# Kernel optimization log

Measured on AMD Instinct MI355X. Metric: run time of the kernel, lower is better.

The kernel has to match this reference:

```python
import jax, jax.numpy as jnp
import numpy as np

N = 4096
D = 256
H = 8
E = 131072
NEG = -1e30  # stands in for -inf; keeps grads NaN-free


def setup_inputs() -> dict:
    key = jax.random.key(0)
    ks = jax.random.split(key, 8)
    s = 1.0 / np.sqrt(D)
    return {
        "x": jax.random.normal(ks[0], (N, D), dtype=jnp.float32),
        "edge_index": jax.random.randint(ks[1], (2, E), 0, N, dtype=jnp.int32),
        "Wq": jax.random.normal(ks[2], (D, D), dtype=jnp.float32) * s,
        "Wk": jax.random.normal(ks[3], (D, D), dtype=jnp.float32) * s,
        "Wv": jax.random.normal(ks[4], (D, D), dtype=jnp.float32) * s,
        "Wo": jax.random.normal(ks[5], (D, D), dtype=jnp.float32) * s,
        "bo": jnp.zeros((D,), dtype=jnp.float32),
        "gamma": jnp.ones((D,), dtype=jnp.float32),
        "beta": jnp.zeros((D,), dtype=jnp.float32),
    }


def reference(x, edge_index, Wq, Wk, Wv, Wo, bo, gamma, beta):
    n, d_model = x.shape
    d_h = d_model // H
    scale = jnp.sqrt(jnp.float32(d_h))

    # mask: True = blocked. Diagonal and graph edges (dst attends to src) unblocked.
    mask = jnp.ones((n, n), dtype=bool)
    diag = jnp.arange(n)
    mask = mask.at[diag, diag].set(False)
    src, dst = edge_index[0], edge_index[1]
    mask = mask.at[dst, src].set(False)

    # projections: torch Linear computes x @ W.T
    Q = (x @ Wq.T).reshape(n, H, d_h).transpose(1, 0, 2)  # [H, N, d_h]
    K = (x @ Wk.T).reshape(n, H, d_h).transpose(1, 0, 2)
    V = (x @ Wv.T).reshape(n, H, d_h).transpose(1, 0, 2)

    scores = jnp.einsum("hnd,hmd->hnm", Q, K) / scale      # [H, N, N]
    scores = jnp.where(mask[None, :, :], NEG, scores)
    attn = jax.nn.softmax(scores, axis=-1)
    attn = jnp.nan_to_num(attn, nan=0.0)

    out = jnp.einsum("hnm,hmd->hnd", attn, V)              # [H, N, d_h]
    out = out.transpose(1, 0, 2).reshape(n, d_model)
    out = out @ Wo.T + bo

    # LayerNorm(x + out), eps=1e-5
    h = x + out
    mu = jnp.mean(h, axis=-1, keepdims=True)
    var = jnp.var(h, axis=-1, keepdims=True)
    return (h - mu) * jax.lax.rsqrt(var + 1e-5) * gamma + beta
```

## Files before the change

kernel.cpp:

```cpp
#include <hip/hip_runtime.h>

#define D_MODEL 256
#define N_HEADS 8
#define MAXN 128
#define NGEMM 384

typedef __attribute__((ext_vector_type(8))) short bf16x8;
typedef __attribute__((ext_vector_type(4))) float f32x4;

#define WSYNC() asm volatile("s_waitcnt lgkmcnt(0)" ::: "memory")

__device__ __forceinline__ unsigned short f2bf(float f) {
    union { float f; unsigned int u; } v; v.f = f;
    unsigned int r = v.u + 0x7fff + ((v.u >> 16) & 1);
    return (unsigned short)(r >> 16);
}
__device__ __forceinline__ float bf2f(unsigned short u) {
    union { unsigned int u; float f; } v; v.u = ((unsigned int)u) << 16;
    return v.f;
}

__global__ void prep_kernel(const float* __restrict__ x,
                            const float* __restrict__ W0, const float* __restrict__ W1,
                            const float* __restrict__ W2, const float* __restrict__ W3,
                            unsigned short* __restrict__ xb,
                            unsigned short* __restrict__ O0, unsigned short* __restrict__ O1,
                            unsigned short* __restrict__ O2, unsigned short* __restrict__ O3,
                            unsigned long long* __restrict__ mask, int n) {
    const int XV = (4096 * 256) / 4;
    int i = blockIdx.x * blockDim.x + threadIdx.x;

    int wpr = n >> 6;
    int mwords = n * wpr;
    if (i < mwords) {
        int row = i >> 6;
        int w = i & 63;
        mask[i] = (w == (row >> 6)) ? (1ULL << (row & 63)) : 0ULL;
    }

    const float* src;
    unsigned short* dst;
    int k;
    if (i < XV) {
        src = x; dst = xb; k = i;
    } else {
        int i2 = i - XV;
        if (i2 >= 4 * 16384) return;
        int z = i2 >> 14;
        k = i2 & 16383;
        src = (z == 0) ? W0 : (z == 1) ? W1 : (z == 2) ? W2 : W3;
        dst = (z == 0) ? O0 : (z == 1) ? O1 : (z == 2) ? O2 : O3;
    }
    float4 v = *(const float4*)(src + (size_t)k * 4);
    ushort4 o;
    o.x = f2bf(v.x); o.y = f2bf(v.y); o.z = f2bf(v.z); o.w = f2bf(v.w);
    *(ushort4*)(dst + (size_t)k * 4) = o;
}

__global__ __launch_bounds__(256) void qkv_edges_kernel(
        const unsigned short* __restrict__ xb,
        const unsigned short* __restrict__ Wq, const unsigned short* __restrict__ Wk,
        const unsigned short* __restrict__ Wv,
        unsigned short* __restrict__ Qb, unsigned short* __restrict__ Kb,
        unsigned short* __restrict__ Vb,
        const int* __restrict__ ei, unsigned long long* __restrict__ mask,
        int E, int n) {
    int blk = blockIdx.x;
    if (blk >= NGEMM) {
        int e = (blk - NGEMM) * 256 + threadIdx.x;
        if (e < E) {
            int src = ei[e];
            int dst = ei[E + e];
            int wpr = n >> 6;
            atomicOr(&mask[(size_t)dst * wpr + (src >> 6)], 1ULL << (src & 63));
        }
        return;
    }
    int z = blk >> 7;
    int r = blk & 127;
    int by = r >> 2, bx = r & 3;
    const unsigned short* B = (z == 0) ? Wq : (z == 1) ? Wk : Wv;
    unsigned short* Cb = (z == 0) ? Qb : (z == 1) ? Kb : Vb;

    __shared__ short Alds[128][72];
    __shared__ short Blds[64][72];
    int t = threadIdx.x;
    int wave = t >> 6, lane = t & 63;
    int wr = wave >> 1, wc = wave & 1;
    int lr = t >> 3;
    int lk = (t & 7) << 3;

    const unsigned short* Abase = xb + ((size_t)(by * 128 + lr)) * D_MODEL + lk;
    const unsigned short* Bbase = B + ((size_t)(bx * 64 + lr)) * D_MODEL + lk;

    int fm = lane & 15;
    int fk = (lane >> 4) << 3;

    f32x4 acc[4][2];
#pragma unroll
    for (int rr = 0; rr < 4; ++rr)
#pragma unroll
        for (int c = 0; c < 2; ++c) acc[rr][c] = (f32x4){0.f, 0.f, 0.f, 0.f};

    for (int k0 = 0; k0 < D_MODEL; k0 += 64) {
        *(uint4*)&Alds[lr][lk]      = *(const uint4*)(Abase + k0);
        *(uint4*)&Alds[lr + 32][lk] = *(const uint4*)(Abase + 32 * D_MODEL + k0);
        *(uint4*)&Alds[lr + 64][lk] = *(const uint4*)(Abase + 64 * D_MODEL + k0);
        *(uint4*)&Alds[lr + 96][lk] = *(const uint4*)(Abase + 96 * D_MODEL + k0);
        *(uint4*)&Blds[lr][lk]      = *(const uint4*)(Bbase + k0);
        *(uint4*)&Blds[lr + 32][lk] = *(const uint4*)(Bbase + 32 * D_MODEL + k0);
        __syncthreads();
#pragma unroll
        for (int ks = 0; ks < 64; ks += 32) {
            bf16x8 af[4], bf[2];
#pragma unroll
            for (int rr = 0; rr < 4; ++rr)
                af[rr] = *(const bf16x8*)&Alds[wr * 64 + rr * 16 + fm][ks + fk];
#pragma unroll
            for (int c = 0; c < 2; ++c)
                bf[c] = *(const bf16x8*)&Blds[wc * 32 + c * 16 + fm][ks + fk];
#pragma unroll
            for (int rr = 0; rr < 4; ++rr)
#pragma unroll
                for (int c = 0; c < 2; ++c)
                    acc[rr][c] = __builtin_amdgcn_mfma_f32_16x16x32_bf16(
                        af[rr], bf[c], acc[rr][c], 0, 0, 0);
        }
        __syncthreads();
    }

    int orow0 = by * 128 + wr * 64 + ((lane >> 4) << 2);
    int ocol0 = bx * 64 + wc * 32 + (lane & 15);
#pragma unroll
    for (int rr = 0; rr < 4; ++rr)
#pragma unroll
        for (int c = 0; c < 2; ++c)
#pragma unroll
            for (int q = 0; q < 4; ++q)
                Cb[(size_t)(orow0 + rr * 16 + q) * D_MODEL + ocol0 + c * 16] =
                    f2bf(acc[rr][c][q]);
}

__global__ __launch_bounds__(256, 8) void attn_kernel(
        const unsigned short* __restrict__ Qb, const unsigned short* __restrict__ Kb,
        const unsigned short* __restrict__ Vb,
        const unsigned long long* __restrict__ mask,
        unsigned short* __restrict__ Ob, int n) {
    __shared__ int nbr_s[4][MAXN + 16];
    __shared__ float s_s[4][N_HEADS][MAXN];

    int t = threadIdx.x;
    int wave = t >> 6, L = t & 63;
    int wpr = n >> 6;
    int dst = blockIdx.x * 4 + wave;

    int* nbrw = nbr_s[wave];
    float (*sw)[MAXN] = s_s[wave];

    unsigned long long w = (L < wpr) ? mask[(size_t)dst * wpr + L] : 0ULL;
    int c = __popcll(w);
    int xs = c;
#pragma unroll
    for (int o = 1; o < 64; o <<= 1) {
        int y = __shfl_up(xs, o, 64);
        if (L >= o) xs += y;
    }
    int pos = xs - c;
    while (w) {
        int b = __builtin_ctzll(w);
        w &= w - 1;
        if (pos < MAXN) nbrw[pos] = (L << 6) + b;
        ++pos;
    }
    int cnt = __shfl(xs, 63, 64);
    if (cnt > MAXN) cnt = MAXN;
    int nb = (cnt + 15) & ~15;
    WSYNC();
    int last = nbrw[cnt - 1];
    if (L < nb - cnt) nbrw[cnt + L] = last;
    WSYNC();

    int col = L & 15;
    int kq = L >> 4;
    bf16x8 qf = (bf16x8){0, 0, 0, 0, 0, 0, 0, 0};
    if (col < N_HEADS)
        qf = *(const bf16x8*)(Qb + (size_t)dst * D_MODEL + col * 32 + kq * 8);
    const bf16x8 zf = (bf16x8){0, 0, 0, 0, 0, 0, 0, 0};
    const float inv_scale = 0.17677669529663687f;

    for (int b0 = 0; b0 < nb; b0 += 16) {
        int nj = nbrw[b0 + col];
        const unsigned short* krow = Kb + (size_t)nj * D_MODEL + kq * 8;
        f32x4 c0 = (f32x4){0.f, 0.f, 0.f, 0.f};
        f32x4 c1 = (f32x4){0.f, 0.f, 0.f, 0.f};
#pragma unroll
        for (int kb = 0; kb < 8; kb += 2) {
            bf16x8 a0 = *(const bf16x8*)(krow + kb * 32);
            bf16x8 a1 = *(const bf16x8*)(krow + kb * 32 + 32);
            bf16x8 bop0 = (col == kb)     ? qf : zf;
            bf16x8 bop1 = (col == kb + 1) ? qf : zf;
            c0 = __builtin_amdgcn_mfma_f32_16x16x32_bf16(a0, bop0, c0, 0, 0, 0);
            c1 = __builtin_amdgcn_mfma_f32_16x16x32_bf16(a1, bop1, c1, 0, 0, 0);
        }
        if (col < N_HEADS) {
            int jr = b0 + kq * 4;
            float4 o4;
            float s0 = (c0[0] + c1[0]) * inv_scale;
            float s1 = (c0[1] + c1[1]) * inv_scale;
            float s2 = (c0[2] + c1[2]) * inv_scale;
            float s3 = (c0[3] + c1[3]) * inv_scale;
            o4.x = (jr + 0 < cnt) ? s0 : -1e30f;
            o4.y = (jr + 1 < cnt) ? s1 : -1e30f;
            o4.z = (jr + 2 < cnt) ? s2 : -1e30f;
            o4.w = (jr + 3 < cnt) ? s3 : -1e30f;
            *(float4*)&sw[col][jr] = o4;
        }
    }
    WSYNC();

    int h = L >> 3, li = L & 7;
    float m = -1e30f;
    for (int j0 = li * 4; j0 < nb; j0 += 32) {
        float4 v = *(const float4*)&sw[h][j0];
        m = fmaxf(m, fmaxf(fmaxf(v.x, v.y), fmaxf(v.z, v.w)));
    }
    m = fmaxf(m, __shfl_xor(m, 1, 8));
    m = fmaxf(m, __shfl_xor(m, 2, 8));
    m = fmaxf(m, __shfl_xor(m, 4, 8));
    float l = 0.f;
    for (int j0 = li * 4; j0 < nb; j0 += 32) {
        float4 v = *(const float4*)&sw[h][j0];
        float4 e4;
        e4.x = __expf(v.x - m); e4.y = __expf(v.y - m);
        e4.z = __expf(v.z - m); e4.w = __expf(v.w - m);
        *(float4*)&sw[h][j0] = e4;
        l += (e4.x + e4.y) + (e4.z + e4.w);
    }
    l += __shfl_xor(l, 1, 8);
    l += __shfl_xor(l, 2, 8);
    l += __shfl_xor(l, 4, 8);
    WSYNC();

    f32x4 acc = (f32x4){0.f, 0.f, 0.f, 0.f};
    const unsigned short* vb = Vb + 4 * L;
    for (int j = 0; j < nb; j += 4) {
        float4 wv = *(const float4*)&sw[h][j];
        int j0 = nbrw[j], j1 = nbrw[j + 1], j2 = nbrw[j + 2], j3 = nbrw[j + 3];
        uint2 r0 = *(const uint2*)(vb + (size_t)j0 * D_MODEL);
        uint2 r1 = *(const uint2*)(vb + (size_t)j1 * D_MODEL);
        uint2 r2 = *(const uint2*)(vb + (size_t)j2 * D_MODEL);
        uint2 r3 = *(const uint2*)(vb + (size_t)j3 * D_MODEL);
        acc[0] += wv.x * bf2f((unsigned short)(r0.x & 0xffff));
        acc[1] += wv.x * bf2f((unsigned short)(r0.x >> 16));
        acc[2] += wv.x * bf2f((unsigned short)(r0.y & 0xffff));
        acc[3] += wv.x * bf2f((unsigned short)(r0.y >> 16));
        acc[0] += wv.y * bf2f((unsigned short)(r1.x & 0xffff));
        acc[1] += wv.y * bf2f((unsigned short)(r1.x >> 16));
        acc[2] += wv.y * bf2f((unsigned short)(r1.y & 0xffff));
        acc[3] += wv.y * bf2f((unsigned short)(r1.y >> 16));
        acc[0] += wv.z * bf2f((unsigned short)(r2.x & 0xffff));
        acc[1] += wv.z * bf2f((unsigned short)(r2.x >> 16));
        acc[2] += wv.z * bf2f((unsigned short)(r2.y & 0xffff));
        acc[3] += wv.z * bf2f((unsigned short)(r2.y >> 16));
        acc[0] += wv.w * bf2f((unsigned short)(r3.x & 0xffff));
        acc[1] += wv.w * bf2f((unsigned short)(r3.x >> 16));
        acc[2] += wv.w * bf2f((unsigned short)(r3.y & 0xffff));
        acc[3] += wv.w * bf2f((unsigned short)(r3.y >> 16));
    }
    float rl = 1.f / l;
    ushort4 o;
    o.x = f2bf(acc[0] * rl); o.y = f2bf(acc[1] * rl);
    o.z = f2bf(acc[2] * rl); o.w = f2bf(acc[3] * rl);
    *(ushort4*)(Ob + (size_t)dst * D_MODEL + 4 * L) = o;
    WSYNC();
}

struct SMemO {
    union {
        struct { short A[32][72]; short B[256][72]; } st;
        float c[32][260];
    };
};

__global__ __launch_bounds__(256) void gemm_o_ln_kernel(
        const unsigned short* __restrict__ Ob, const unsigned short* __restrict__ Wob,
        const float* __restrict__ x, const float* __restrict__ bo,
        const float* __restrict__ gamma, const float* __restrict__ beta,
        float* __restrict__ out) {
    __shared__ SMemO sm;
    int by = blockIdx.x;
    int t = threadIdx.x;
    int wave = t >> 6, lane = t & 63;
    int rt = wave >> 1, cq = wave & 1;
    int lr = t >> 3;
    int lk = (t & 7) << 3;

    const unsigned short* Abase = Ob + ((size_t)(by * 32 + lr)) * D_MODEL + lk;
    int fm = lane & 15;
    int fk = (lane >> 4) << 3;

    f32x4 acc[8];
#pragma unroll
    for (int ct = 0; ct < 8; ++ct) acc[ct] = (f32x4){0.f, 0.f, 0.f, 0.f};

    for (int k0 = 0; k0 < D_MODEL; k0 += 64) {
        *(uint4*)&sm.st.A[lr][lk] = *(const uint4*)(Abase + k0);
#pragma unroll
        for (int j = 0; j < 8; ++j)
            *(uint4*)&sm.st.B[lr + 32 * j][lk] =
                *(const uint4*)(Wob + ((size_t)(lr + 32 * j)) * D_MODEL + k0 + lk);
        __syncthreads();
#pragma unroll
        for (int ks = 0; ks < 64; ks += 32) {
            bf16x8 af = *(const bf16x8*)&sm.st.A[rt * 16 + fm][ks + fk];
#pragma unroll
            for (int ct = 0; ct < 8; ++ct) {
                bf16x8 bf = *(const bf16x8*)&sm.st.B[cq * 128 + ct * 16 + fm][ks + fk];
                acc[ct] = __builtin_amdgcn_mfma_f32_16x16x32_bf16(af, bf, acc[ct], 0, 0, 0);
            }
        }
        __syncthreads();
    }

    int rr0 = rt * 16 + ((lane >> 4) << 2);
#pragma unroll
    for (int ct = 0; ct < 8; ++ct)
#pragma unroll
        for (int q = 0; q < 4; ++q)
            sm.c[rr0 + q][cq * 128 + ct * 16 + (lane & 15)] = acc[ct][q];
    __syncthreads();

    float4 bo4 = *(const float4*)(bo + lane * 4);
    float4 g4  = *(const float4*)(gamma + lane * 4);
    float4 be4 = *(const float4*)(beta + lane * 4);
#pragma unroll
    for (int rr = 0; rr < 8; ++rr) {
        int r = wave * 8 + rr;
        int grow = by * 32 + r;
        float4 p = *(const float4*)&sm.c[r][lane * 4];
        float4 xv = *(const float4*)(x + (size_t)grow * D_MODEL + lane * 4);
        float hx = p.x + xv.x + bo4.x;
        float hy = p.y + xv.y + bo4.y;
        float hz = p.z + xv.z + bo4.z;
        float hw = p.w + xv.w + bo4.w;
        float s  = (hx + hy) + (hz + hw);
        float s2 = (hx * hx + hy * hy) + (hz * hz + hw * hw);
#pragma unroll
        for (int o = 32; o; o >>= 1) {
            s  += __shfl_xor(s, o, 64);
            s2 += __shfl_xor(s2, o, 64);
        }
        float mu = s * (1.f / 256.f);
        float var = s2 * (1.f / 256.f) - mu * mu;
        float rstd = rsqrtf(var + 1e-5f);
        float4 o4;
        o4.x = (hx - mu) * rstd * g4.x + be4.x;
        o4.y = (hy - mu) * rstd * g4.y + be4.y;
        o4.z = (hz - mu) * rstd * g4.z + be4.z;
        o4.w = (hw - mu) * rstd * g4.w + be4.w;
        *(float4*)(out + (size_t)grow * D_MODEL + lane * 4) = o4;
    }
}

extern "C" void kernel_launch(void* const* d_in, const int* in_sizes, int n_in,
                              void* d_out, int out_size, void* d_ws, size_t ws_size,
                              hipStream_t stream) {
    const float* x     = (const float*)d_in[0];
    const int*   ei    = (const int*)  d_in[1];
    const float* Wq    = (const float*)d_in[2];
    const float* Wk    = (const float*)d_in[3];
    const float* Wv    = (const float*)d_in[4];
    const float* Wo    = (const float*)d_in[5];
    const float* bo    = (const float*)d_in[6];
    const float* gamma = (const float*)d_in[7];
    const float* beta  = (const float*)d_in[8];
    float* out = (float*)d_out;

    int n = in_sizes[0] / D_MODEL;
    int E = in_sizes[1] / 2;

    char* ws = (char*)d_ws;
    size_t off = 0;
    unsigned long long* mask = (unsigned long long*)(ws + off);
    off += (size_t)n * (n >> 6) * sizeof(unsigned long long);
    unsigned short* xb  = (unsigned short*)(ws + off); off += (size_t)n * D_MODEL * 2;
    unsigned short* Wqb = (unsigned short*)(ws + off); off += D_MODEL * D_MODEL * 2;
    unsigned short* Wkb = (unsigned short*)(ws + off); off += D_MODEL * D_MODEL * 2;
    unsigned short* Wvb = (unsigned short*)(ws + off); off += D_MODEL * D_MODEL * 2;
    unsigned short* Wob = (unsigned short*)(ws + off); off += D_MODEL * D_MODEL * 2;
    unsigned short* Qb  = (unsigned short*)(ws + off); off += (size_t)n * D_MODEL * 2;
    unsigned short* Kb  = (unsigned short*)(ws + off); off += (size_t)n * D_MODEL * 2;
    unsigned short* Vb  = (unsigned short*)(ws + off); off += (size_t)n * D_MODEL * 2;
    unsigned short* Ob  = (unsigned short*)(ws + off); off += (size_t)n * D_MODEL * 2;

    prep_kernel<<<1280, 256, 0, stream>>>(x, Wq, Wk, Wv, Wo,
                                          xb, Wqb, Wkb, Wvb, Wob, mask, n);

    int edge_blocks = (E + 255) / 256;
    qkv_edges_kernel<<<NGEMM + edge_blocks, 256, 0, stream>>>(
        xb, Wqb, Wkb, Wvb, Qb, Kb, Vb, ei, mask, E, n);

    attn_kernel<<<n / 4, 256, 0, stream>>>(Qb, Kb, Vb, mask, Ob, n);

    gemm_o_ln_kernel<<<n / 32, 256, 0, stream>>>(Ob, Wob, x, bo, gamma, beta, out);
}
```

Measured before the change: 114.1 us.

## Retile QKV and output GEMMs and restructure attention gather loops

The QKV GEMM now stages 128-wide K slices, so it runs half as many k-iterations and barriers. In the attention kernel, all eight K fragments are loaded up front and spread across four MFMA accumulators to shorten the dependency chain. The V gather now uses 16-byte loads, with two half-waves each taking alternate neighbours and combining through a cross-lane shuffle, and occupancy hints are lowered. The output GEMM+LayerNorm uses 16-row tiles to double the block count, at the cost of reloading Wo into LDS more often overall.

```diff
diff --git a/kernel.cpp b/kernel.cpp
--- a/kernel.cpp
+++ b/kernel.cpp
@@ -82,16 +82,13 @@
     const unsigned short* B = (z == 0) ? Wq : (z == 1) ? Wk : Wv;
     unsigned short* Cb = (z == 0) ? Qb : (z == 1) ? Kb : Vb;
 
-    __shared__ short Alds[128][72];
-    __shared__ short Blds[64][72];
+    __shared__ short Alds[128][136];
+    __shared__ short Blds[64][136];
     int t = threadIdx.x;
     int wave = t >> 6, lane = t & 63;
     int wr = wave >> 1, wc = wave & 1;
-    int lr = t >> 3;
-    int lk = (t & 7) << 3;
-
-    const unsigned short* Abase = xb + ((size_t)(by * 128 + lr)) * D_MODEL + lk;
-    const unsigned short* Bbase = B + ((size_t)(bx * 64 + lr)) * D_MODEL + lk;
+    int lrA = t >> 4;
+    int lc = (t & 15) << 3;
 
     int fm = lane & 15;
     int fk = (lane >> 4) << 3;
@@ -102,16 +99,18 @@
 #pragma unroll
         for (int c = 0; c < 2; ++c) acc[rr][c] = (f32x4){0.f, 0.f, 0.f, 0.f};
 
-    for (int k0 = 0; k0 < D_MODEL; k0 += 64) {
-        *(uint4*)&Alds[lr][lk]      = *(const uint4*)(Abase + k0);
-        *(uint4*)&Alds[lr + 32][lk] = *(const uint4*)(Abase + 32 * D_MODEL + k0);
-        *(uint4*)&Alds[lr + 64][lk] = *(const uint4*)(Abase + 64 * D_MODEL + k0);
-        *(uint4*)&Alds[lr + 96][lk] = *(const uint4*)(Abase + 96 * D_MODEL + k0);
-        *(uint4*)&Blds[lr][lk]      = *(const uint4*)(Bbase + k0);
-        *(uint4*)&Blds[lr + 32][lk] = *(const uint4*)(Bbase + 32 * D_MODEL + k0);
+    for (int k0 = 0; k0 < D_MODEL; k0 += 128) {
+#pragma unroll
+        for (int i = 0; i < 8; ++i)
+            *(uint4*)&Alds[lrA + 16 * i][lc] =
+                *(const uint4*)(xb + ((size_t)(by * 128 + lrA + 16 * i)) * D_MODEL + k0 + lc);
+#pragma unroll
+        for (int i = 0; i < 4; ++i)
+            *(uint4*)&Blds[lrA + 16 * i][lc] =
+                *(const uint4*)(B + ((size_t)(bx * 64 + lrA + 16 * i)) * D_MODEL + k0 + lc);
         __syncthreads();
 #pragma unroll
-        for (int ks = 0; ks < 64; ks += 32) {
+        for (int ks = 0; ks < 128; ks += 32) {
             bf16x8 af[4], bf[2];
 #pragma unroll
             for (int rr = 0; rr < 4; ++rr)
@@ -141,13 +140,14 @@
                     f2bf(acc[rr][c][q]);
 }
 
-__global__ __launch_bounds__(256, 8) void attn_kernel(
+__global__ __launch_bounds__(256, 4) void attn_kernel(
         const unsigned short* __restrict__ Qb, const unsigned short* __restrict__ Kb,
         const unsigned short* __restrict__ Vb,
         const unsigned long long* __restrict__ mask,
         unsigned short* __restrict__ Ob, int n) {
     __shared__ int nbr_s[4][MAXN + 16];
     __shared__ float s_s[4][N_HEADS][MAXN];
+    __shared__ float lsum_s[4][N_HEADS];
 
     int t = threadIdx.x;
     int wave = t >> 6, L = t & 63;
@@ -191,24 +191,29 @@
     for (int b0 = 0; b0 < nb; b0 += 16) {
         int nj = nbrw[b0 + col];
         const unsigned short* krow = Kb + (size_t)nj * D_MODEL + kq * 8;
+        bf16x8 a[8];
+#pragma unroll
+        for (int kb = 0; kb < 8; ++kb)
+            a[kb] = *(const bf16x8*)(krow + kb * 32);
         f32x4 c0 = (f32x4){0.f, 0.f, 0.f, 0.f};
         f32x4 c1 = (f32x4){0.f, 0.f, 0.f, 0.f};
-#pragma unroll
-        for (int kb = 0; kb < 8; kb += 2) {
-            bf16x8 a0 = *(const bf16x8*)(krow + kb * 32);
-            bf16x8 a1 = *(const bf16x8*)(krow + kb * 32 + 32);
-            bf16x8 bop0 = (col == kb)     ? qf : zf;
-            bf16x8 bop1 = (col == kb + 1) ? qf : zf;
-            c0 = __builtin_amdgcn_mfma_f32_16x16x32_bf16(a0, bop0, c0, 0, 0, 0);
-            c1 = __builtin_amdgcn_mfma_f32_16x16x32_bf16(a1, bop1, c1, 0, 0, 0);
-        }
+        f32x4 c2 = (f32x4){0.f, 0.f, 0.f, 0.f};
+        f32x4 c3 = (f32x4){0.f, 0.f, 0.f, 0.f};
+        c0 = __builtin_amdgcn_mfma_f32_16x16x32_bf16(a[0], (col == 0) ? qf : zf, c0, 0, 0, 0);
+        c1 = __builtin_amdgcn_mfma_f32_16x16x32_bf16(a[1], (col == 1) ? qf : zf, c1, 0, 0, 0);
+        c2 = __builtin_amdgcn_mfma_f32_16x16x32_bf16(a[2], (col == 2) ? qf : zf, c2, 0, 0, 0);
+        c3 = __builtin_amdgcn_mfma_f32_16x16x32_bf16(a[3], (col == 3) ? qf : zf, c3, 0, 0, 0);
+        c0 = __builtin_amdgcn_mfma_f32_16x16x32_bf16(a[4], (col == 4) ? qf : zf, c0, 0, 0, 0);
+        c1 = __builtin_amdgcn_mfma_f32_16x16x32_bf16(a[5], (col == 5) ? qf : zf, c1, 0, 0, 0);
+        c2 = __builtin_amdgcn_mfma_f32_16x16x32_bf16(a[6], (col == 6) ? qf : zf, c2, 0, 0, 0);
+        c3 = __builtin_amdgcn_mfma_f32_16x16x32_bf16(a[7], (col == 7) ? qf : zf, c3, 0, 0, 0);
         if (col < N_HEADS) {
             int jr = b0 + kq * 4;
             float4 o4;
-            float s0 = (c0[0] + c1[0]) * inv_scale;
-            float s1 = (c0[1] + c1[1]) * inv_scale;
-            float s2 = (c0[2] + c1[2]) * inv_scale;
-            float s3 = (c0[3] + c1[3]) * inv_scale;
+            float s0 = ((c0[0] + c1[0]) + (c2[0] + c3[0])) * inv_scale;
+            float s1 = ((c0[1] + c1[1]) + (c2[1] + c3[1])) * inv_scale;
+            float s2 = ((c0[2] + c1[2]) + (c2[2] + c3[2])) * inv_scale;
+            float s3 = ((c0[3] + c1[3]) + (c2[3] + c3[3])) * inv_scale;
             o4.x = (jr + 0 < cnt) ? s0 : -1e30f;
             o4.y = (jr + 1 < cnt) ? s1 : -1e30f;
             o4.z = (jr + 2 < cnt) ? s2 : -1e30f;
@@ -239,46 +244,57 @@
     l += __shfl_xor(l, 1, 8);
     l += __shfl_xor(l, 2, 8);
     l += __shfl_xor(l, 4, 8);
+    if (li == 0) lsum_s[wave][h] = l;
     WSYNC();
 
-    f32x4 acc = (f32x4){0.f, 0.f, 0.f, 0.f};
-    const unsigned short* vb = Vb + 4 * L;
-    for (int j = 0; j < nb; j += 4) {
-        float4 wv = *(const float4*)&sw[h][j];
-        int j0 = nbrw[j], j1 = nbrw[j + 1], j2 = nbrw[j + 2], j3 = nbrw[j + 3];
-        uint2 r0 = *(const uint2*)(vb + (size_t)j0 * D_MODEL);
-        uint2 r1 = *(const uint2*)(vb + (size_t)j1 * D_MODEL);
-        uint2 r2 = *(const uint2*)(vb + (size_t)j2 * D_MODEL);
-        uint2 r3 = *(const uint2*)(vb + (size_t)j3 * D_MODEL);
-        acc[0] += wv.x * bf2f((unsigned short)(r0.x & 0xffff));
-        acc[1] += wv.x * bf2f((unsigned short)(r0.x >> 16));
-        acc[2] += wv.x * bf2f((unsigned short)(r0.y & 0xffff));
-        acc[3] += wv.x * bf2f((unsigned short)(r0.y >> 16));
-        acc[0] += wv.y * bf2f((unsigned short)(r1.x & 0xffff));
-        acc[1] += wv.y * bf2f((unsigned short)(r1.x >> 16));
-        acc[2] += wv.y * bf2f((unsigned short)(r1.y & 0xffff));
-        acc[3] += wv.y * bf2f((unsigned short)(r1.y >> 16));
-        acc[0] += wv.z * bf2f((unsigned short)(r2.x & 0xffff));
-        acc[1] += wv.z * bf2f((unsigned short)(r2.x >> 16));
-        acc[2] += wv.z * bf2f((unsigned short)(r2.y & 0xffff));
-        acc[3] += wv.z * bf2f((unsigned short)(r2.y >> 16));
-        acc[0] += wv.w * bf2f((unsigned short)(r3.x & 0xffff));
-        acc[1] += wv.w * bf2f((unsigned short)(r3.x >> 16));
-        acc[2] += wv.w * bf2f((unsigned short)(r3.y & 0xffff));
-        acc[3] += wv.w * bf2f((unsigned short)(r3.y >> 16));
-    }
-    float rl = 1.f / l;
-    ushort4 o;
-    o.x = f2bf(acc[0] * rl); o.y = f2bf(acc[1] * rl);
-    o.z = f2bf(acc[2] * rl); o.w = f2bf(acc[3] * rl);
-    *(ushort4*)(Ob + (size_t)dst * D_MODEL + 4 * L) = o;
-    WSYNC();
+    int H = L >> 5, l5 = L & 31;
+    int hsel = l5 >> 2;
+    float rl = 1.f / lsum_s[wave][hsel];
+    f32x4 accA = (f32x4){0.f, 0.f, 0.f, 0.f};
+    f32x4 accB = (f32x4){0.f, 0.f, 0.f, 0.f};
+    const unsigned short* vb = Vb + 8 * l5;
+    for (int j = 0; j < nb; j += 8) {
+        int j0 = nbrw[j + 0 + H], j1 = nbrw[j + 2 + H];
+        int j2 = nbrw[j + 4 + H], j3 = nbrw[j + 6 + H];
+        float w0 = sw[hsel][j + 0 + H], w1 = sw[hsel][j + 2 + H];
+        float w2 = sw[hsel][j + 4 + H], w3 = sw[hsel][j + 6 + H];
+        uint4 r0 = *(const uint4*)(vb + (size_t)j0 * D_MODEL);
+        uint4 r1 = *(const uint4*)(vb + (size_t)j1 * D_MODEL);
+        uint4 r2 = *(const uint4*)(vb + (size_t)j2 * D_MODEL);
+        uint4 r3 = *(const uint4*)(vb + (size_t)j3 * D_MODEL);
+#define ACC8(rr, ww) \
+        accA[0] += ww * bf2f((unsigned short)(rr.x & 0xffff)); \
+        accA[1] += ww * bf2f((unsigned short)(rr.x >> 16));    \
+        accA[2] += ww * bf2f((unsigned short)(rr.y & 0xffff)); \
+        accA[3] += ww * bf2f((unsigned short)(rr.y >> 16));    \
+        accB[0] += ww * bf2f((unsigned short)(rr.z & 0xffff)); \
+        accB[1] += ww * bf2f((unsigned short)(rr.z >> 16));    \
+        accB[2] += ww * bf2f((unsigned short)(rr.w & 0xffff)); \
+        accB[3] += ww * bf2f((unsigned short)(rr.w >> 16));
+        ACC8(r0, w0) ACC8(r1, w1) ACC8(r2, w2) ACC8(r3, w3)
+#undef ACC8
+    }
+#pragma unroll
+    for (int q = 0; q < 4; ++q) {
+        accA[q] = (accA[q] + __shfl_xor(accA[q], 32, 64)) * rl;
+        accB[q] = (accB[q] + __shfl_xor(accB[q], 32, 64)) * rl;
+    }
+    if (H == 0) {
+        ushort4 oa, ob;
+        oa.x = f2bf(accA[0]); oa.y = f2bf(accA[1]);
+        oa.z = f2bf(accA[2]); oa.w = f2bf(accA[3]);
+        ob.x = f2bf(accB[0]); ob.y = f2bf(accB[1]);
+        ob.z = f2bf(accB[2]); ob.w = f2bf(accB[3]);
+        unsigned short* op = Ob + (size_t)dst * D_MODEL + 8 * l5;
+        *(ushort4*)op = oa;
+        *(ushort4*)(op + 4) = ob;
+    }
 }
 
 struct SMemO {
     union {
-        struct { short A[32][72]; short B[256][72]; } st;
-        float c[32][260];
+        struct { short A[16][72]; short B[256][72]; } st;
+        float c[16][260];
     };
 };
 
@@ -291,52 +307,53 @@
     int by = blockIdx.x;
     int t = threadIdx.x;
     int wave = t >> 6, lane = t & 63;
-    int rt = wave >> 1, cq = wave & 1;
-    int lr = t >> 3;
-    int lk = (t & 7) << 3;
-
-    const unsigned short* Abase = Ob + ((size_t)(by * 32 + lr)) * D_MODEL + lk;
     int fm = lane & 15;
     int fk = (lane >> 4) << 3;
 
-    f32x4 acc[8];
-#pragma unroll
-    for (int ct = 0; ct < 8; ++ct) acc[ct] = (f32x4){0.f, 0.f, 0.f, 0.f};
+    int lrB = t >> 3;
+    int lcB = (t & 7) << 3;
+    int lrA = t >> 4;
+    int lcA = (t & 15) << 2;
+
+    f32x4 acc[4];
+#pragma unroll
+    for (int ct = 0; ct < 4; ++ct) acc[ct] = (f32x4){0.f, 0.f, 0.f, 0.f};
 
     for (int k0 = 0; k0 < D_MODEL; k0 += 64) {
-        *(uint4*)&sm.st.A[lr][lk] = *(const uint4*)(Abase + k0);
+        *(uint2*)&sm.st.A[lrA][lcA] =
+            *(const uint2*)(Ob + ((size_t)(by * 16 + lrA)) * D_MODEL + k0 + lcA);
 #pragma unroll
         for (int j = 0; j < 8; ++j)
-            *(uint4*)&sm.st.B[lr + 32 * j][lk] =
-                *(const uint4*)(Wob + ((size_t)(lr + 32 * j)) * D_MODEL + k0 + lk);
+            *(uint4*)&sm.st.B[lrB + 32 * j][lcB] =
+                *(const uint4*)(Wob + ((size_t)(lrB + 32 * j)) * D_MODEL + k0 + lcB);
         __syncthreads();
 #pragma unroll
         for (int ks = 0; ks < 64; ks += 32) {
-            bf16x8 af = *(const bf16x8*)&sm.st.A[rt * 16 + fm][ks + fk];
-#pragma unroll
-            for (int ct = 0; ct < 8; ++ct) {
-                bf16x8 bf = *(const bf16x8*)&sm.st.B[cq * 128 + ct * 16 + fm][ks + fk];
+            bf16x8 af = *(const bf16x8*)&sm.st.A[fm][ks + fk];
+#pragma unroll
+            for (int ct = 0; ct < 4; ++ct) {
+                bf16x8 bf = *(const bf16x8*)&sm.st.B[wave * 64 + ct * 16 + fm][ks + fk];
                 acc[ct] = __builtin_amdgcn_mfma_f32_16x16x32_bf16(af, bf, acc[ct], 0, 0, 0);
             }
         }
         __syncthreads();
     }
 
-    int rr0 = rt * 16 + ((lane >> 4) << 2);
-#pragma unroll
-    for (int ct = 0; ct < 8; ++ct)
+    int rr0 = (lane >> 4) << 2;
+#pragma unroll
+    for (int ct = 0; ct < 4; ++ct)
 #pragma unroll
         for (int q = 0; q < 4; ++q)
-            sm.c[rr0 + q][cq * 128 + ct * 16 + (lane & 15)] = acc[ct][q];
+            sm.c[rr0 + q][wave * 64 + ct * 16 + (lane & 15)] = acc[ct][q];
     __syncthreads();
 
     float4 bo4 = *(const float4*)(bo + lane * 4);
     float4 g4  = *(const float4*)(gamma + lane * 4);
     float4 be4 = *(const float4*)(beta + lane * 4);
 #pragma unroll
-    for (int rr = 0; rr < 8; ++rr) {
-        int r = wave * 8 + rr;
-        int grow = by * 32 + r;
+    for (int rr = 0; rr < 4; ++rr) {
+        int r = wave * 4 + rr;
+        int grow = by * 16 + r;
         float4 p = *(const float4*)&sm.c[r][lane * 4];
         float4 xv = *(const float4*)(x + (size_t)grow * D_MODEL + lane * 4);
         float hx = p.x + xv.x + bo4.x;
@@ -402,5 +419,5 @@
 
     attn_kernel<<<n / 4, 256, 0, stream>>>(Qb, Kb, Vb, mask, Ob, n);
 
-    gemm_o_ln_kernel<<<n / 32, 256, 0, stream>>>(Ob, Wob, x, bo, gamma, beta, out);
-}
+    gemm_o_ln_kernel<<<n / 16, 256, 0, stream>>>(Ob, Wob, x, bo, gamma, beta, out);
+}
```

Result: no change. 116.0 us (+1.7%).
